# Kernel optimization log

Measured on AMD Instinct MI355X. Metric: run time of the kernel, lower is better.

The kernel has to match this reference:

```python
import jax, jax.numpy as jnp
import numpy as np

D_MODEL = 256
NUM_HEADS = 8
DIM_HEAD = D_MODEL // NUM_HEADS
EPS = 1e-6
MASK_BIAS = -1.0e9


def setup_inputs() -> dict:
    key = jax.random.key(0)
    ks = jax.random.split(key, 10)
    B, S = 2, 4096
    x = jax.random.normal(ks[0], (B, S, D_MODEL), dtype=jnp.float32)
    pad_mask = jnp.zeros((B, S), dtype=jnp.float32)  # 1.0 => padded position
    scale = 1.0 / np.sqrt(D_MODEL)
    Wq = jax.random.normal(ks[1], (D_MODEL, D_MODEL), dtype=jnp.float32) * scale
    bq = jnp.zeros((D_MODEL,), dtype=jnp.float32)
    Wk = jax.random.normal(ks[2], (D_MODEL, D_MODEL), dtype=jnp.float32) * scale
    bk = jnp.zeros((D_MODEL,), dtype=jnp.float32)
    Wv = jax.random.normal(ks[3], (D_MODEL, D_MODEL), dtype=jnp.float32) * scale
    bv = jnp.zeros((D_MODEL,), dtype=jnp.float32)
    gamma = jnp.ones((D_MODEL,), dtype=jnp.float32)
    beta = jnp.zeros((D_MODEL,), dtype=jnp.float32)
    return {"x": x, "pad_mask": pad_mask, "Wq": Wq, "bq": bq, "Wk": Wk,
            "bk": bk, "Wv": Wv, "bv": bv, "gamma": gamma, "beta": beta}


def _layer_norm(h, gamma, beta):
    mu = jnp.mean(h, axis=-1, keepdims=True)
    var = jnp.mean(jnp.square(h - mu), axis=-1, keepdims=True)
    return gamma * (h - mu) * jax.lax.rsqrt(var + EPS) + beta


def reference(x, pad_mask, Wq, bq, Wk, bk, Wv, bv, gamma, beta):
    B, S, D = x.shape
    q = x @ Wq + bq  # [B,S,D]
    k = x @ Wk + bk
    v = x @ Wv + bv
    # split heads: [B,S,D] -> [B,H,S,Dh]
    def split(t):
        return t.reshape(B, S, NUM_HEADS, DIM_HEAD).transpose(0, 2, 1, 3)
    qh, kh, vh = split(q), split(k), split(v)
    w = jnp.einsum("bhqd,bhkd->bhqk", qh, kh)  # [B,H,S,S]
    # faithful to source: mask added BEFORE the 1/sqrt(dim_head) scaling
    w = w + pad_mask[:, None, None, :] * MASK_BIAS
    w = w / jnp.sqrt(jnp.float32(DIM_HEAD))
    attn = jax.nn.softmax(w, axis=-1)
    # dropout is identity at inference
    out = jnp.einsum("bhqk,bhkd->bhqd", attn, vh)  # [B,H,S,Dh]
    out = out.transpose(0, 2, 1, 3).reshape(B, S, D)
    return _layer_norm(out + x, gamma, beta)
```

## Files before the change

### kernel.cpp

```cpp
#include <hip/hip_runtime.h>
#include <hip/hip_bf16.h>

#define D_MODEL 256
#define NUM_HEADS 8
#define DIM_HEAD 32
#define SEQ 4096
#define BATCH 2
#define NROWS (BATCH * SEQ)
#define LN_EPS 1e-6f
#define MASK_BIAS -1.0e9f
#define SCALE 0.17677669529663687f
#define LOG2E 1.4426950408889634f

typedef __attribute__((ext_vector_type(8))) short short8;
typedef __attribute__((ext_vector_type(4))) float f32x4;

static __device__ __forceinline__ unsigned short f2b(float f) {
    union { __hip_bfloat16 b; unsigned short u; } cv;
    cv.b = __float2bfloat16(f);
    return cv.u;
}
static __device__ __forceinline__ unsigned int pk_bf16(float lo, float hi) {
    union { __hip_bfloat162 v; unsigned int u; } cv;
    cv.v = __float22bfloat162_rn(make_float2(lo, hi));
    return cv.u;
}
static __device__ __forceinline__ float exp2_raw(float x) {
#if __has_builtin(__builtin_amdgcn_exp2f)
    return __builtin_amdgcn_exp2f(x);
#else
    float r;
    asm volatile("v_exp_f32 %0, %1" : "=v"(r) : "v"(x));
    return r;
#endif
}
static __device__ __forceinline__ void load_lds16(const void* g, void* l) {
    __builtin_amdgcn_global_load_lds(
        (const __attribute__((address_space(1))) unsigned int*)g,
        (__attribute__((address_space(3))) unsigned int*)l, 16, 0, 0);
}

__global__ __launch_bounds__(256) void prep_kernel(
    const float* __restrict__ Wq, const float* __restrict__ Wk,
    const float* __restrict__ Wv,
    const float* __restrict__ bq, const float* __restrict__ bk,
    const float* __restrict__ bv,
    const float* __restrict__ pad,
    unsigned short* __restrict__ Wt, float* __restrict__ biasc,
    float* __restrict__ T2)
{
    const int blk = blockIdx.x;
    const int t = threadIdx.x;
    if (blk < 768) {
        const int w = blk >> 8;
        const int k = blk & 255;
        const float* W = (w == 0) ? Wq : (w == 1) ? Wk : Wv;
        Wt[(size_t)(w * 256 + t) * 256 + k] = f2b(W[(size_t)k * 256 + t]);
        if (k == 0) {
            const float* bb = (w == 0) ? bq : (w == 1) ? bk : bv;
            biasc[w * 256 + t] = bb[t];
        }
    } else {
        const int i = (blk - 768) * 256 + t;
        T2[i] = pad[i] * (MASK_BIAS * SCALE * LOG2E);
    }
}

__global__ __launch_bounds__(256) void qkv_mfma_kernel(
    const float* __restrict__ x, const unsigned short* __restrict__ Wt,
    const float* __restrict__ biasc,
    unsigned short* __restrict__ Qh, unsigned short* __restrict__ Kh,
    unsigned short* __restrict__ Vt)
{
    const int lane = threadIdx.x & 63;
    const int wid  = threadIdx.x >> 6;
    const int c    = lane & 15;
    const int quad = lane >> 4;

    const int r0 = (blockIdx.x >> 3) * 64 + wid * 16;
    const int n0 = (blockIdx.x & 7) * 96;

    f32x4 acc[6];
    float bias[6];
    #pragma unroll
    for (int t = 0; t < 6; t++) {
        acc[t] = (f32x4){0.f, 0.f, 0.f, 0.f};
        bias[t] = biasc[n0 + 16 * t + c];
    }

    const float* xp0 = x + (size_t)(r0 + c) * D_MODEL + quad * 8;
    const unsigned short* wp0 = Wt + (size_t)(n0 + c) * 256 + quad * 8;

    for (int k0 = 0; k0 < 256; k0 += 32) {
        const float4 a0 = *(const float4*)(xp0 + k0);
        const float4 a1 = *(const float4*)(xp0 + k0 + 4);
        union { unsigned int u[4]; short8 s; } af;
        af.u[0] = pk_bf16(a0.x, a0.y);
        af.u[1] = pk_bf16(a0.z, a0.w);
        af.u[2] = pk_bf16(a1.x, a1.y);
        af.u[3] = pk_bf16(a1.z, a1.w);
        #pragma unroll
        for (int t = 0; t < 6; t++) {
            const short8 bf = *(const short8*)(wp0 + (size_t)(16 * t) * 256 + k0);
            acc[t] = __builtin_amdgcn_mfma_f32_16x16x32_bf16(af.s, bf, acc[t], 0, 0, 0);
        }
    }

    #pragma unroll
    for (int t = 0; t < 6; t++) {
        const int col = n0 + 16 * t;
        const int mm  = col >> 8;
        const int dim = (col & 255) + c;
        const int h = dim >> 5, d = dim & 31;
        const int row = r0 + quad * 4;
        const int bb = row >> 12;
        const int s  = row & (SEQ - 1);
        const size_t bh = (size_t)(bb * NUM_HEADS + h);
        const float v0 = acc[t][0] + bias[t];
        const float v1 = acc[t][1] + bias[t];
        const float v2 = acc[t][2] + bias[t];
        const float v3 = acc[t][3] + bias[t];
        if (mm == 2) {
            uint2 pk = make_uint2(pk_bf16(v0, v1), pk_bf16(v2, v3));
            *(uint2*)(Vt + (bh * DIM_HEAD + d) * SEQ + s) = pk;
        } else {
            unsigned short* P = (mm == 0 ? Qh : Kh) + (bh * SEQ + s) * DIM_HEAD + d;
            P[0]  = f2b(v0);
            P[32] = f2b(v1);
            P[64] = f2b(v2);
            P[96] = f2b(v3);
        }
    }
}

__global__ __launch_bounds__(256, 4) void attn_mfma_kernel(
    const unsigned short* __restrict__ Qh, const unsigned short* __restrict__ Kh,
    const unsigned short* __restrict__ Vt, const float* __restrict__ T2,
    float* __restrict__ O)
{
    __shared__ __align__(16) unsigned short ldsK[2][64 * 32];
    __shared__ __align__(16) unsigned short ldsV[2][32 * 64];
    __shared__ __align__(16) float          ldsT[2][64];

    const int lane = threadIdx.x & 63;
    const int wid  = threadIdx.x >> 6;
    const int c    = lane & 15;
    const int quad = lane >> 4;

    const int gw = blockIdx.x;
    const int q0 = (gw & 63) * 64;
    const int h  = (gw >> 6) & (NUM_HEADS - 1);
    const int b  = gw >> 9;
    const size_t bh = (size_t)(b * NUM_HEADS + h);

    const float k2 = SCALE * LOG2E;
    const int perm = ((c & 12) << 1) | (c & 3);

    const unsigned short* Kb = Kh + bh * SEQ * DIM_HEAD;
    const unsigned short* Vb = Vt + bh * DIM_HEAD * SEQ;
    const float* Tb = T2 + (size_t)b * SEQ;

    const int qrow = q0 + wid * 16;
    const short8 qf = *(const short8*)(Qh + (bh * SEQ + qrow + c) * DIM_HEAD + quad * 8);

    union { unsigned int u[4]; short8 s; } ones;
    ones.u[0] = ones.u[1] = ones.u[2] = ones.u[3] = 0x3F803F80u;

    const int f0 = ((perm >> 1) ^ (perm >> 3)) & 3;
    const int f1 = (((perm + 4) >> 1) ^ ((perm + 4) >> 3)) & 3;
    const int kA = perm * 32 + ((quad ^ f0) << 3);
    const int kB = (perm + 4) * 32 + ((quad ^ f1) << 3);
    const int g0 = quad ^ (c & 7);
    const int vA0 = c * 64 + (g0 << 3);
    const int vA1 = c * 64 + ((g0 ^ 4) << 3);
    const int vB0 = (16 + c) * 64 + (g0 << 3);
    const int vB1 = (16 + c) * 64 + ((g0 ^ 4) << 3);

    const int skey = (lane >> 2);
    const int sgK  = lane & 3;
    const int sdim = lane >> 3;
    const int sgV  = lane & 7;

    f32x4 o0 = {0.f,0.f,0.f,0.f}, o1 = {0.f,0.f,0.f,0.f};
    f32x4 lacc = {0.f,0.f,0.f,0.f};
    const f32x4 z = {0.f, 0.f, 0.f, 0.f};

    auto stage = [&](int ch, int pb) {
        const int s0 = ch * 64;
        if (wid < 2) {
            #pragma unroll
            for (int jj = 0; jj < 2; jj++) {
                const int j = wid * 2 + jj;
                const int key = j * 16 + skey;
                const int f = ((key >> 1) ^ (key >> 3)) & 3;
                load_lds16(Kb + (size_t)(s0 + key) * 32 + ((sgK ^ f) << 3),
                           &ldsK[pb][j * 512]);
            }
        } else {
            #pragma unroll
            for (int jj = 0; jj < 2; jj++) {
                const int j = (wid - 2) * 2 + jj;
                const int dim = j * 8 + sdim;
                load_lds16(Vb + (size_t)dim * SEQ + s0 + ((sgV ^ (dim & 7)) << 3),
                           &ldsV[pb][j * 512]);
            }
            if (wid == 3 && lane < 16)
                load_lds16(Tb + s0 + lane * 4, &ldsT[pb][0]);
        }
    };

    auto sub = [&](int pb, int s) {
        const short8 kf0 = *(const short8*)&ldsK[pb][s * 1024 + kA];
        const short8 kf1 = *(const short8*)&ldsK[pb][s * 1024 + kB];
        const short8 vf0 = *(const short8*)&ldsV[pb][s ? vA1 : vA0];
        const short8 vf1 = *(const short8*)&ldsV[pb][s ? vB1 : vB0];
        const float4 t0 = *(const float4*)&ldsT[pb][s * 32 + quad * 8];
        const float4 t1 = *(const float4*)&ldsT[pb][s * 32 + quad * 8 + 4];

        const f32x4 st0 = __builtin_amdgcn_mfma_f32_16x16x32_bf16(kf0, qf, z, 0, 0, 0);
        const f32x4 st1 = __builtin_amdgcn_mfma_f32_16x16x32_bf16(kf1, qf, z, 0, 0, 0);

        float p[8];
        p[0] = exp2_raw(fmaf(st0[0], k2, t0.x));
        p[1] = exp2_raw(fmaf(st0[1], k2, t0.y));
        p[2] = exp2_raw(fmaf(st0[2], k2, t0.z));
        p[3] = exp2_raw(fmaf(st0[3], k2, t0.w));
        p[4] = exp2_raw(fmaf(st1[0], k2, t1.x));
        p[5] = exp2_raw(fmaf(st1[1], k2, t1.y));
        p[6] = exp2_raw(fmaf(st1[2], k2, t1.z));
        p[7] = exp2_raw(fmaf(st1[3], k2, t1.w));

        union { unsigned int u[4]; short8 s8; } pf;
        pf.u[0] = pk_bf16(p[0], p[1]);
        pf.u[1] = pk_bf16(p[2], p[3]);
        pf.u[2] = pk_bf16(p[4], p[5]);
        pf.u[3] = pk_bf16(p[6], p[7]);

        lacc = __builtin_amdgcn_mfma_f32_16x16x32_bf16(ones.s, pf.s8, lacc, 0, 0, 0);
        o0   = __builtin_amdgcn_mfma_f32_16x16x32_bf16(vf0,   pf.s8, o0,   0, 0, 0);
        o1   = __builtin_amdgcn_mfma_f32_16x16x32_bf16(vf1,   pf.s8, o1,   0, 0, 0);
    };

    stage(0, 0);
    __syncthreads();
    for (int ch = 0; ch < SEQ / 64; ++ch) {
        const int pb = ch & 1;
        stage((ch + 1) & 63, pb ^ 1);
        sub(pb, 0);
        sub(pb, 1);
        __syncthreads();
    }

    const float inv = 1.0f / lacc[0];
    float* op = O + ((size_t)(b * SEQ) + qrow + c) * D_MODEL + h * DIM_HEAD + quad * 4;
    *(float4*)op        = make_float4(o0[0]*inv, o0[1]*inv, o0[2]*inv, o0[3]*inv);
    *(float4*)(op + 16) = make_float4(o1[0]*inv, o1[1]*inv, o1[2]*inv, o1[3]*inv);
}

__global__ __launch_bounds__(256) void ln_kernel(
    float* AO,
    const float* __restrict__ x,
    const float* __restrict__ gamma, const float* __restrict__ beta)
{
    const int lane = threadIdx.x & 63;
    const int wid  = threadIdx.x >> 6;
    const size_t row = (size_t)blockIdx.x * 4 + wid;

    const float4 a  = ((const float4*)(AO + row * D_MODEL))[lane];
    const float4 xv = ((const float4*)(x + row * D_MODEL))[lane];
    float hv[4];
    hv[0] = a.x + xv.x;
    hv[1] = a.y + xv.y;
    hv[2] = a.z + xv.z;
    hv[3] = a.w + xv.w;

    float s = hv[0] + hv[1] + hv[2] + hv[3];
    #pragma unroll
    for (int off = 32; off > 0; off >>= 1) s += __shfl_xor(s, off, 64);
    const float mu = s * (1.0f / D_MODEL);

    float d0 = hv[0]-mu, d1 = hv[1]-mu, d2 = hv[2]-mu, d3 = hv[3]-mu;
    float ss = d0*d0 + d1*d1 + d2*d2 + d3*d3;
    #pragma unroll
    for (int off = 32; off > 0; off >>= 1) ss += __shfl_xor(ss, off, 64);
    const float rs = rsqrtf(ss * (1.0f / D_MODEL) + LN_EPS);

    const float4 g  = ((const float4*)gamma)[lane];
    const float4 bb = ((const float4*)beta)[lane];
    float4 y;
    y.x = g.x * d0 * rs + bb.x;
    y.y = g.y * d1 * rs + bb.y;
    y.z = g.z * d2 * rs + bb.z;
    y.w = g.w * d3 * rs + bb.w;
    ((float4*)(AO + row * D_MODEL))[lane] = y;
}

extern "C" void kernel_launch(void* const* d_in, const int* in_sizes, int n_in,
                              void* d_out, int out_size, void* d_ws, size_t ws_size,
                              hipStream_t stream)
{
    const float* x     = (const float*)d_in[0];
    const float* pad   = (const float*)d_in[1];
    const float* Wq    = (const float*)d_in[2];
    const float* bq    = (const float*)d_in[3];
    const float* Wk    = (const float*)d_in[4];
    const float* bk    = (const float*)d_in[5];
    const float* Wv    = (const float*)d_in[6];
    const float* bv    = (const float*)d_in[7];
    const float* gamma = (const float*)d_in[8];
    const float* beta  = (const float*)d_in[9];

    const size_t elems = (size_t)NROWS * D_MODEL;
    unsigned short* Qh = (unsigned short*)d_ws;
    unsigned short* Kh = Qh + elems;
    unsigned short* Vt = Kh + elems;
    float* T2 = (float*)(Vt + elems);
    unsigned short* Wt = (unsigned short*)(T2 + NROWS);
    float* biasc = (float*)(Wt + 768 * 256);
    float* AO = (float*)d_out;

    prep_kernel<<<800, 256, 0, stream>>>(Wq, Wk, Wv, bq, bk, bv, pad,
                                         Wt, biasc, T2);
    qkv_mfma_kernel<<<(NROWS / 64) * 8, 256, 0, stream>>>(x, Wt, biasc,
                                                          Qh, Kh, Vt);
    attn_mfma_kernel<<<BATCH * NUM_HEADS * (SEQ / 64), 256, 0, stream>>>(
        Qh, Kh, Vt, T2, AO);
    ln_kernel<<<NROWS / 4, 256, 0, stream>>>(AO, x, gamma, beta);
}
```

Baseline: 188.8 us.

## Split attention over key halves and merge partial sums in layernorm

The attention kernel now splits each query tile's key range into two halves across separate blocks. It writes unnormalized partial outputs and row sums to workspace, and the layernorm kernel combines them. This doubles the grid and raises the occupancy hint to get more parallelism. The softmax has no running max, so the partials add directly. The QKV projection is retiled to 64-column blocks, with a transposed MFMA for Q/K so each lane writes packed 4-element stores. The cost is extra global traffic for the second partial buffer and the sums.

Measured after the change: 198.7 us. +5.2%, slower.

```diff
diff --git a/kernel.cpp b/kernel.cpp
--- a/kernel.cpp
+++ b/kernel.cpp
@@ -77,66 +77,84 @@
     const int c    = lane & 15;
     const int quad = lane >> 4;
 
-    const int r0 = (blockIdx.x >> 3) * 64 + wid * 16;
-    const int n0 = (blockIdx.x & 7) * 96;
-
-    f32x4 acc[6];
-    float bias[6];
+    const int rb = blockIdx.x / 12;
+    const int cb = blockIdx.x % 12;
+    const int r0 = rb * 64 + wid * 16;
+    const int n0 = cb * 64;
+    const bool isV = (n0 >= 512);
+
+    f32x4 acc[4];
     #pragma unroll
-    for (int t = 0; t < 6; t++) {
-        acc[t] = (f32x4){0.f, 0.f, 0.f, 0.f};
-        bias[t] = biasc[n0 + 16 * t + c];
-    }
+    for (int t = 0; t < 4; t++) acc[t] = (f32x4){0.f, 0.f, 0.f, 0.f};
 
     const float* xp0 = x + (size_t)(r0 + c) * D_MODEL + quad * 8;
     const unsigned short* wp0 = Wt + (size_t)(n0 + c) * 256 + quad * 8;
 
-    for (int k0 = 0; k0 < 256; k0 += 32) {
-        const float4 a0 = *(const float4*)(xp0 + k0);
-        const float4 a1 = *(const float4*)(xp0 + k0 + 4);
-        union { unsigned int u[4]; short8 s; } af;
-        af.u[0] = pk_bf16(a0.x, a0.y);
-        af.u[1] = pk_bf16(a0.z, a0.w);
-        af.u[2] = pk_bf16(a1.x, a1.y);
-        af.u[3] = pk_bf16(a1.z, a1.w);
+    if (!isV) {
+        for (int k0 = 0; k0 < 256; k0 += 32) {
+            const float4 a0 = *(const float4*)(xp0 + k0);
+            const float4 a1 = *(const float4*)(xp0 + k0 + 4);
+            union { unsigned int u[4]; short8 s; } af;
+            af.u[0] = pk_bf16(a0.x, a0.y);
+            af.u[1] = pk_bf16(a0.z, a0.w);
+            af.u[2] = pk_bf16(a1.x, a1.y);
+            af.u[3] = pk_bf16(a1.z, a1.w);
+            #pragma unroll
+            for (int t = 0; t < 4; t++) {
+                const short8 bf = *(const short8*)(wp0 + (size_t)(16 * t) * 256 + k0);
+                acc[t] = __builtin_amdgcn_mfma_f32_16x16x32_bf16(bf, af.s, acc[t], 0, 0, 0);
+            }
+        }
+        const int row = r0 + c;
+        const int bb = row >> 12;
+        const int s  = row & (SEQ - 1);
+        unsigned short* base = (n0 < 256) ? Qh : Kh;
         #pragma unroll
-        for (int t = 0; t < 6; t++) {
-            const short8 bf = *(const short8*)(wp0 + (size_t)(16 * t) * 256 + k0);
-            acc[t] = __builtin_amdgcn_mfma_f32_16x16x32_bf16(af.s, bf, acc[t], 0, 0, 0);
-        }
-    }
-
-    #pragma unroll
-    for (int t = 0; t < 6; t++) {
-        const int col = n0 + 16 * t;
-        const int mm  = col >> 8;
-        const int dim = (col & 255) + c;
-        const int h = dim >> 5, d = dim & 31;
+        for (int t = 0; t < 4; t++) {
+            const int dim = (n0 & 255) + 16 * t + quad * 4;
+            const int h = dim >> 5, d = dim & 31;
+            const float4 b4 = *(const float4*)(biasc + n0 + 16 * t + quad * 4);
+            const size_t bh = (size_t)(bb * NUM_HEADS + h);
+            uint2 pk = make_uint2(pk_bf16(acc[t][0] + b4.x, acc[t][1] + b4.y),
+                                  pk_bf16(acc[t][2] + b4.z, acc[t][3] + b4.w));
+            *(uint2*)(base + (bh * SEQ + s) * DIM_HEAD + d) = pk;
+        }
+    } else {
+        for (int k0 = 0; k0 < 256; k0 += 32) {
+            const float4 a0 = *(const float4*)(xp0 + k0);
+            const float4 a1 = *(const float4*)(xp0 + k0 + 4);
+            union { unsigned int u[4]; short8 s; } af;
+            af.u[0] = pk_bf16(a0.x, a0.y);
+            af.u[1] = pk_bf16(a0.z, a0.w);
+            af.u[2] = pk_bf16(a1.x, a1.y);
+            af.u[3] = pk_bf16(a1.z, a1.w);
+            #pragma unroll
+            for (int t = 0; t < 4; t++) {
+                const short8 bf = *(const short8*)(wp0 + (size_t)(16 * t) * 256 + k0);
+                acc[t] = __builtin_amdgcn_mfma_f32_16x16x32_bf16(af.s, bf, acc[t], 0, 0, 0);
+            }
+        }
         const int row = r0 + quad * 4;
         const int bb = row >> 12;
         const int s  = row & (SEQ - 1);
-        const size_t bh = (size_t)(bb * NUM_HEADS + h);
-        const float v0 = acc[t][0] + bias[t];
-        const float v1 = acc[t][1] + bias[t];
-        const float v2 = acc[t][2] + bias[t];
-        const float v3 = acc[t][3] + bias[t];
-        if (mm == 2) {
-            uint2 pk = make_uint2(pk_bf16(v0, v1), pk_bf16(v2, v3));
+        #pragma unroll
+        for (int t = 0; t < 4; t++) {
+            const int dim = (n0 & 255) + 16 * t + c;
+            const int h = dim >> 5, d = dim & 31;
+            const float bv = biasc[n0 + 16 * t + c];
+            const size_t bh = (size_t)(bb * NUM_HEADS + h);
+            uint2 pk = make_uint2(pk_bf16(acc[t][0] + bv, acc[t][1] + bv),
+                                  pk_bf16(acc[t][2] + bv, acc[t][3] + bv));
             *(uint2*)(Vt + (bh * DIM_HEAD + d) * SEQ + s) = pk;
-        } else {
-            unsigned short* P = (mm == 0 ? Qh : Kh) + (bh * SEQ + s) * DIM_HEAD + d;
-            P[0]  = f2b(v0);
-            P[32] = f2b(v1);
-            P[64] = f2b(v2);
-            P[96] = f2b(v3);
         }
     }
 }
 
-__global__ __launch_bounds__(256, 4) void attn_mfma_kernel(
+__global__ __launch_bounds__(256, 8) void attn_mfma_kernel(
     const unsigned short* __restrict__ Qh, const unsigned short* __restrict__ Kh,
     const unsigned short* __restrict__ Vt, const float* __restrict__ T2,
-    float* __restrict__ O)
+    float* __restrict__ P1, float* __restrict__ P2,
+    float* __restrict__ L1, float* __restrict__ L2)
 {
     __shared__ __align__(16) unsigned short ldsK[2][64 * 32];
     __shared__ __align__(16) unsigned short ldsV[2][32 * 64];
@@ -148,9 +166,10 @@
     const int quad = lane >> 4;
 
     const int gw = blockIdx.x;
-    const int q0 = (gw & 63) * 64;
-    const int h  = (gw >> 6) & (NUM_HEADS - 1);
-    const int b  = gw >> 9;
+    const int e  = gw & 1;
+    const int q0 = ((gw >> 1) & 63) * 64;
+    const int h  = (gw >> 7) & (NUM_HEADS - 1);
+    const int b  = gw >> 10;
     const size_t bh = (size_t)(b * NUM_HEADS + h);
 
     const float k2 = SCALE * LOG2E;
@@ -159,6 +178,7 @@
     const unsigned short* Kb = Kh + bh * SEQ * DIM_HEAD;
     const unsigned short* Vb = Vt + bh * DIM_HEAD * SEQ;
     const float* Tb = T2 + (size_t)b * SEQ;
+    const int sbase = e * (SEQ / 2);
 
     const int qrow = q0 + wid * 16;
     const short8 qf = *(const short8*)(Qh + (bh * SEQ + qrow + c) * DIM_HEAD + quad * 8);
@@ -185,8 +205,8 @@
     f32x4 lacc = {0.f,0.f,0.f,0.f};
     const f32x4 z = {0.f, 0.f, 0.f, 0.f};
 
-    auto stage = [&](int ch, int pb) {
-        const int s0 = ch * 64;
+    auto stage = [&](int lch, int pb) {
+        const int s0 = sbase + lch * 64;
         if (wid < 2) {
             #pragma unroll
             for (int jj = 0; jj < 2; jj++) {
@@ -243,36 +263,46 @@
 
     stage(0, 0);
     __syncthreads();
-    for (int ch = 0; ch < SEQ / 64; ++ch) {
+    for (int ch = 0; ch < 32; ++ch) {
         const int pb = ch & 1;
-        stage((ch + 1) & 63, pb ^ 1);
+        stage((ch + 1) & 31, pb ^ 1);
         sub(pb, 0);
         sub(pb, 1);
         __syncthreads();
     }
 
-    const float inv = 1.0f / lacc[0];
-    float* op = O + ((size_t)(b * SEQ) + qrow + c) * D_MODEL + h * DIM_HEAD + quad * 4;
-    *(float4*)op        = make_float4(o0[0]*inv, o0[1]*inv, o0[2]*inv, o0[3]*inv);
-    *(float4*)(op + 16) = make_float4(o1[0]*inv, o1[1]*inv, o1[2]*inv, o1[3]*inv);
+    float* Pe = e ? P2 : P1;
+    float* op = Pe + ((size_t)(b * SEQ) + qrow + c) * D_MODEL + h * DIM_HEAD + quad * 4;
+    *(float4*)op        = make_float4(o0[0], o0[1], o0[2], o0[3]);
+    *(float4*)(op + 16) = make_float4(o1[0], o1[1], o1[2], o1[3]);
+    if (quad == 0) {
+        float* Le = e ? L2 : L1;
+        Le[((size_t)(b * SEQ) + qrow + c) * NUM_HEADS + h] = lacc[0];
+    }
 }
 
 __global__ __launch_bounds__(256) void ln_kernel(
-    float* AO,
+    float* P1,
+    const float* __restrict__ P2,
+    const float* __restrict__ L1, const float* __restrict__ L2,
     const float* __restrict__ x,
     const float* __restrict__ gamma, const float* __restrict__ beta)
 {
     const int lane = threadIdx.x & 63;
     const int wid  = threadIdx.x >> 6;
     const size_t row = (size_t)blockIdx.x * 4 + wid;
-
-    const float4 a  = ((const float4*)(AO + row * D_MODEL))[lane];
+    const int h = lane >> 3;
+
+    const float4 a  = ((const float4*)(P1 + row * D_MODEL))[lane];
+    const float4 p2 = ((const float4*)(P2 + row * D_MODEL))[lane];
     const float4 xv = ((const float4*)(x + row * D_MODEL))[lane];
+    const float inv = 1.0f / (L1[row * NUM_HEADS + h] + L2[row * NUM_HEADS + h]);
+
     float hv[4];
-    hv[0] = a.x + xv.x;
-    hv[1] = a.y + xv.y;
-    hv[2] = a.z + xv.z;
-    hv[3] = a.w + xv.w;
+    hv[0] = (a.x + p2.x) * inv + xv.x;
+    hv[1] = (a.y + p2.y) * inv + xv.y;
+    hv[2] = (a.z + p2.z) * inv + xv.z;
+    hv[3] = (a.w + p2.w) * inv + xv.w;
 
     float s = hv[0] + hv[1] + hv[2] + hv[3];
     #pragma unroll
@@ -292,7 +322,7 @@
     y.y = g.y * d1 * rs + bb.y;
     y.z = g.z * d2 * rs + bb.z;
     y.w = g.w * d3 * rs + bb.w;
-    ((float4*)(AO + row * D_MODEL))[lane] = y;
+    ((float4*)(P1 + row * D_MODEL))[lane] = y;
 }
 
 extern "C" void kernel_launch(void* const* d_in, const int* in_sizes, int n_in,
@@ -317,13 +347,16 @@
     float* T2 = (float*)(Vt + elems);
     unsigned short* Wt = (unsigned short*)(T2 + NROWS);
     float* biasc = (float*)(Wt + 768 * 256);
-    float* AO = (float*)d_out;
+    float* P2 = biasc + 768;
+    float* L1 = P2 + elems;
+    float* L2 = L1 + (size_t)NROWS * NUM_HEADS;
+    float* P1 = (float*)d_out;
 
     prep_kernel<<<800, 256, 0, stream>>>(Wq, Wk, Wv, bq, bk, bv, pad,
                                          Wt, biasc, T2);
-    qkv_mfma_kernel<<<(NROWS / 64) * 8, 256, 0, stream>>>(x, Wt, biasc,
-                                                          Qh, Kh, Vt);
-    attn_mfma_kernel<<<BATCH * NUM_HEADS * (SEQ / 64), 256, 0, stream>>>(
-        Qh, Kh, Vt, T2, AO);
-    ln_kernel<<<NROWS / 4, 256, 0, stream>>>(AO, x, gamma, beta);
-}
+    qkv_mfma_kernel<<<(NROWS / 64) * 12, 256, 0, stream>>>(x, Wt, biasc,
+                                                           Qh, Kh, Vt);
+    attn_mfma_kernel<<<BATCH * NUM_HEADS * (SEQ / 64) * 2, 256, 0, stream>>>(
+        Qh, Kh, Vt, T2, P1, P2, L1, L2);
+    ln_kernel<<<NROWS / 4, 256, 0, stream>>>(P1, P2, L1, L2, x, gamma, beta);
+}
```
